# Kernel tuning notes

Hardware: AMD Instinct MI355X
Metric: run time of the kernel (lower is better)

## Reference

```python
import jax, jax.numpy as jnp
import numpy as np

# Model dims: nSet=48, nItemMax=80, input feat=512,
# D = baseChn*max_channel_ratio = 128 = head_size, H = num_heads = 2.
S, N, DIN = 48, 80, 512
D = 128
H, HS = 2, 128
EPS = 1e-3  # layer_normalization epsilon (non-set-norm branch)

def _w(key, fi, fo):
    return jax.random.normal(key, (fi, fo), jnp.float32) / np.sqrt(fi)

def setup_inputs() -> dict:
    key = jax.random.key(0)
    ks = jax.random.split(key, 20)
    sizes = jax.random.randint(ks[0], (S,), 1, N + 1)
    x = jax.random.normal(ks[1], (S, N, DIN), jnp.float32)
    item_mask = (jnp.arange(N)[None, :] < sizes[:, None]).astype(jnp.float32)
    x = x * item_mask[:, :, None]  # zero-pad invalid items (drives ==0 masks)
    return {
        "x": x,
        "x_size": sizes.astype(jnp.float32),
        # trainable MLP (fc1/fc2/fc3, gelu, no bias)
        "W1": _w(ks[2], DIN, 512),
        "W2": _w(ks[3], 512, 256),
        "W3": _w(ks[4], 256, D),
        # encoder self-attention layer
        "Wq_s": _w(ks[5], D, H * HS),
        "Wk_s": _w(ks[6], D, H * HS),
        "Wv_s": _w(ks[7], D, H * HS),
        "Wh_s": _w(ks[8], H * HS, HS),
        "Wfc_e": _w(ks[9], D, D),
        # decoder cross-set attention layer
        "Wq_c": _w(ks[10], D, H * HS),
        "Wk_c": _w(ks[11], D, H * HS),
        "Wv_c": _w(ks[12], D, H * HS),
        "Wh_c": _w(ks[13], H * HS, HS),
        "Wfc_d": _w(ks[14], D, D),
        # cross_set_score
        "Wcs": _w(ks[15], D, H * HS),
        "Wcs2": _w(ks[16], H, 1),
    }

def _gelu(z):
    return jax.nn.gelu(z, approximate=False)  # tf.nn.gelu default

def _item_norm(x):
    # layer_normalization with is_set_norm=False: per-item LN, zero padded rows
    mean = jnp.mean(x, axis=-1, keepdims=True)
    std = jnp.std(x, axis=-1, keepdims=True)
    norm = (x - mean) / (std + EPS)
    keep = jnp.sum(x, axis=-1, keepdims=True) != 0
    return jnp.where(keep, norm, jnp.zeros_like(x))

def _masked_softmax(s):
    # faithful to source: mask entries where raw score == 0
    m = s != 0
    e = jnp.where(m, jnp.exp(s - jnp.max(s, axis=-1, keepdims=True)), 0.0)
    return e / (jnp.sum(e, axis=-1, keepdims=True) + 1e-10)

def _mha(q_in, kv_in, Wq, Wk, Wv, Wh):
    # q_in/kv_in: [S, S, N, D]
    q = (q_in @ Wq).reshape(S, S, N, H, HS)
    k = (kv_in @ Wk).reshape(S, S, N, H, HS)
    v = (kv_in @ Wv).reshape(S, S, N, H, HS)
    s = jnp.einsum('xynhd,xymhd->xyhnm', q, k) / np.sqrt(HS)
    a = _masked_softmax(s)
    o = jnp.einsum('xyhnm,xymhd->xynhd', a, v).reshape(S, S, N, H * HS)
    return o @ Wh  # -> [S, S, N, HS]

def reference(x, x_size, W1, W2, W3, Wq_s, Wk_s, Wv_s, Wh_s, Wfc_e,
              Wq_c, Wk_c, Wv_c, Wh_c, Wfc_d, Wcs, Wcs2):
    # item-wise MLP projection: feat -> 512 -> 256 -> 128
    h = _gelu(_gelu(_gelu(x @ W1) @ W2) @ W3)  # [S, N, D]
    # pairwise set grid [nSet_x, nSet_y, nItemMax, D]
    x4 = jnp.broadcast_to(h[:, None], (S, S, N, D))
    # encoder: self-attention over items within each (i,j) pair
    z = _item_norm(x4)
    x4 = x4 + _mha(z, z, Wq_s, Wk_s, Wv_s, Wh_s)
    z = _item_norm(x4)
    x4 = x4 + _gelu(z @ Wfc_e)
    # decoder: cross-set attention, out[i,j] = Attn(q=z[i,j], kv=z[j,i])
    z = _item_norm(x4)
    x4 = x4 + _mha(z, jnp.transpose(z, (1, 0, 2, 3)), Wq_c, Wk_c, Wv_c, Wh_c)
    z = _item_norm(x4)
    x4 = x4 + _gelu(z @ Wfc_d)
    # cross_set_score: pairwise ReLU-matmul, set-size normalized
    xh = (x4 @ Wcs).reshape(S, S, N, H, HS).transpose(0, 1, 3, 2, 4)  # [j,i,h,n,d]
    A = jax.nn.relu(jnp.einsum('jihnd,ijhmd->jihnm', xh, xh) / np.sqrt(HS))
    sc = A.sum((-1, -2)) / x_size[None, :, None] / x_size[:, None, None]  # [S,S,H]
    return sc @ Wcs2  # [S, S, 1]
```

## Files before the change

kernel.cpp:

```cpp
#include <hip/hip_runtime.h>
#include <hip/hip_bf16.h>


#define SS 48
#define NI 80

typedef unsigned short us;
typedef __attribute__((ext_vector_type(8))) short s8v;
typedef __attribute__((ext_vector_type(4))) float f4v;

#define MFMA(a,b,c) __builtin_amdgcn_mfma_f32_16x16x32_bf16((a),(b),(c),0,0,0)

__device__ __forceinline__ float gelu_f(float x){
  return 0.5f * x * (1.0f + erff(x * 0.7071067811865475f));
}
__device__ __forceinline__ us f2b(float f){
  __hip_bfloat16 b = __float2bfloat16(f);
  return reinterpret_cast<us&>(b);
}
__device__ __forceinline__ s8v zero8(){ s8v v = {0,0,0,0,0,0,0,0}; return v; }
__device__ __forceinline__ void gl16(const void* g, void* l){
  __builtin_amdgcn_global_load_lds(
      (const __attribute__((address_space(1))) void*)g,
      (__attribute__((address_space(3))) void*)l, 16, 0, 0);
}

template<int ABF16, int OUTF32>
__global__ __launch_bounds__(256) void mgemm_k(const void* __restrict__ Ap,
    const float* __restrict__ B, void* __restrict__ Cp, int N, int K)
{
  __shared__ __align__(16) char lds[10240];
  char* As = lds; char* Bs = lds + 5120;
  const int t = threadIdx.x;
  const int wv = t >> 6, lm = t & 15, lh = (t >> 4) & 3;
  const int bx = blockIdx.x, by = blockIdx.y;
  const int ar = wv*16 + lm, r0 = wv*16 + lh*4;
  f4v acc[4];
#pragma unroll
  for (int ct = 0; ct < 4; ++ct) acc[ct] = {0.f,0.f,0.f,0.f};
  const int rA = t >> 2, kcA = (t & 3) << 3;
  const int kkB = t >> 3, nnB = (t & 7) << 3;
  for (int k0 = 0; k0 < K; k0 += 32) {
    __syncthreads();
    if (ABF16) {
      s8v v = *(const s8v*)((const us*)Ap + (size_t)(by*64 + rA)*K + k0 + kcA);
      *(s8v*)(As + rA*80 + kcA*2) = v;
    } else {
      const float* ap = (const float*)Ap + (size_t)(by*64 + rA)*K + k0 + kcA;
      float4 v0 = *(const float4*)ap, v1 = *(const float4*)(ap + 4);
      us tmp[8] = {f2b(v0.x),f2b(v0.y),f2b(v0.z),f2b(v0.w),
                   f2b(v1.x),f2b(v1.y),f2b(v1.z),f2b(v1.w)};
      *(s8v*)(As + rA*80 + kcA*2) = *(const s8v*)tmp;
    }
    {
      const float* bp = B + (size_t)(k0 + kkB)*N + bx*64 + nnB;
      float4 w0 = *(const float4*)bp, w1 = *(const float4*)(bp + 4);
      float w8[8] = {w0.x,w0.y,w0.z,w0.w,w1.x,w1.y,w1.z,w1.w};
#pragma unroll
      for (int q = 0; q < 8; ++q)
        *(us*)(Bs + (nnB + q)*80 + kkB*2) = f2b(w8[q]);
    }
    __syncthreads();
    s8v af = *(const s8v*)(As + ar*80 + lh*16);
#pragma unroll
    for (int ct = 0; ct < 4; ++ct) {
      s8v bf = *(const s8v*)(Bs + (ct*16 + lm)*80 + lh*16);
      acc[ct] = MFMA(af, bf, acc[ct]);
    }
  }
#pragma unroll
  for (int ct = 0; ct < 4; ++ct)
#pragma unroll
    for (int reg = 0; reg < 4; ++reg) {
      size_t r = by*64 + r0 + reg;
      int c = bx*64 + ct*16 + lm;
      float v = gelu_f(acc[ct][reg]);
      if (OUTF32) ((float*)Cp)[r*N + c] = v;
      else ((us*)Cp)[r*N + c] = f2b(v);
    }
}

__global__ __launch_bounds__(256) void qkv_k(const us* __restrict__ A,
    const float* __restrict__ Wq, const float* __restrict__ Wk,
    const float* __restrict__ Wv, us* __restrict__ Qb, us* __restrict__ Kb,
    us* __restrict__ VT)
{
  __shared__ __align__(16) char lds[10240];
  char* As = lds; char* Bs = lds + 5120;
  const int t = threadIdx.x;
  const int wv = t >> 6, lm = t & 15, lh = (t >> 4) & 3;
  const int bx = blockIdx.x, by = blockIdx.y;
  const int sel = bx >> 2, bxx = bx & 3;
  const float* B = sel == 0 ? Wq : (sel == 1 ? Wk : Wv);
  const int ar = wv*16 + lm, r0 = wv*16 + lh*4;
  f4v acc[4];
#pragma unroll
  for (int ct = 0; ct < 4; ++ct) acc[ct] = {0.f,0.f,0.f,0.f};
  const int rA = t >> 2, kcA = (t & 3) << 3;
  const int kkB = t >> 3, nnB = (t & 7) << 3;
#pragma unroll
  for (int k0 = 0; k0 < 128; k0 += 32) {
    __syncthreads();
    {
      s8v v = *(const s8v*)(A + (size_t)(by*64 + rA)*128 + k0 + kcA);
      *(s8v*)(As + rA*80 + kcA*2) = v;
      const float* bp = B + (size_t)(k0 + kkB)*256 + bxx*64 + nnB;
      float4 w0 = *(const float4*)bp, w1 = *(const float4*)(bp + 4);
      float w8[8] = {w0.x,w0.y,w0.z,w0.w,w1.x,w1.y,w1.z,w1.w};
#pragma unroll
      for (int q = 0; q < 8; ++q)
        *(us*)(Bs + (nnB + q)*80 + kkB*2) = f2b(w8[q]);
    }
    __syncthreads();
    s8v af = *(const s8v*)(As + ar*80 + lh*16);
#pragma unroll
    for (int ct = 0; ct < 4; ++ct) {
      s8v bf = *(const s8v*)(Bs + (ct*16 + lm)*80 + lh*16);
      acc[ct] = MFMA(af, bf, acc[ct]);
    }
  }
  if (sel < 2) {
    us* O = sel ? Kb : Qb;
#pragma unroll
    for (int ct = 0; ct < 4; ++ct)
#pragma unroll
      for (int reg = 0; reg < 4; ++reg)
        O[(size_t)(by*64 + r0 + reg)*256 + bxx*64 + ct*16 + lm] = f2b(acc[ct][reg]);
  } else {
#pragma unroll
    for (int ct = 0; ct < 4; ++ct)
#pragma unroll
      for (int reg = 0; reg < 4; ++reg) {
        int r = by*64 + r0 + reg;
        int s = r / 80, m = r % 80;
        int d = bxx*64 + ct*16 + lm;
        VT[((size_t)s*256 + d)*80 + m] = f2b(acc[ct][reg]);
      }
  }
}

__global__ __launch_bounds__(64) void norm_k(const float* __restrict__ in,
                                             us* __restrict__ out)
{
  const int r = blockIdx.x, t = threadIdx.x;
  float v0 = in[(size_t)r*128 + t];
  float v1 = in[(size_t)r*128 + t + 64];
  float sm = v0 + v1;
#pragma unroll
  for (int off = 1; off < 64; off <<= 1) sm += __shfl_xor(sm, off, 64);
  float mean = sm * (1.0f/128.0f);
  float d0 = v0 - mean, d1 = v1 - mean;
  float vs = d0*d0 + d1*d1;
#pragma unroll
  for (int off = 1; off < 64; off <<= 1) vs += __shfl_xor(vs, off, 64);
  float inv = 1.0f / (sqrtf(vs * (1.0f/128.0f)) + 1e-3f);
  bool keep = (sm != 0.0f);
  out[(size_t)r*128 + t]      = f2b(keep ? d0*inv : 0.0f);
  out[(size_t)r*128 + t + 64] = f2b(keep ? d1*inv : 0.0f);
}

__global__ __launch_bounds__(128) void prep_k(
    const float* __restrict__ Wh_s, const float* __restrict__ Wfc_e,
    const float* __restrict__ Wh_c, const float* __restrict__ Wfc_d,
    const float* __restrict__ Wcs,  const float* __restrict__ Wv_s,
    const float* __restrict__ Wv_c,
    us* __restrict__ WfcTe, us* __restrict__ WfcTd,
    float* __restrict__ Wvh_s, float* __restrict__ Wvh_c,
    us* __restrict__ Mb)
{
  const int x = blockIdx.x, task = blockIdx.y, tid = threadIdx.x;
  if (task == 0) {
    WfcTe[x*128 + tid] = f2b(Wfc_e[(size_t)tid*128 + x]);
  } else if (task == 1) {
    WfcTd[x*128 + tid] = f2b(Wfc_d[(size_t)tid*128 + x]);
  } else if (task < 6) {
    int h = (task - 2) & 1;
    const float* Wv = task < 4 ? Wv_s : Wv_c;
    const float* Wh = task < 4 ? Wh_s : Wh_c;
    float* Wvh = task < 4 ? Wvh_s : Wvh_c;
    float acc = 0.f;
#pragma unroll 8
    for (int d = 0; d < 128; ++d)
      acc = fmaf(Wv[(size_t)x*256 + h*128 + d], Wh[(size_t)(h*128 + d)*128 + tid], acc);
    Wvh[(size_t)x*256 + h*128 + tid] = acc;
  } else {
    int h = task - 6;
    float acc = 0.f;
#pragma unroll 8
    for (int k = 0; k < 128; ++k)
      acc = fmaf(Wcs[(size_t)x*256 + h*128 + k], Wcs[(size_t)tid*256 + h*128 + k], acc);
    Mb[(size_t)h*16384 + x*128 + tid] = f2b(acc);
  }
}

template<int PERM_RES>
__device__ __forceinline__ void attn4(int a, int b, int t,
    const us* __restrict__ Qg, const us* __restrict__ Kg,
    const us* __restrict__ VTg, const float* __restrict__ baseg,
    const us* __restrict__ WfcT,
    char* __restrict__ X, char* __restrict__ Y, f4v x4[8])
{
  const int wv = t >> 6, lane = t & 63, lm = t & 15, lh = (t >> 4) & 3;
  const int ar = wv*16 + lm, r0 = wv*16 + lh*4;
  const float isq = 0.08838834764831845f;
#pragma unroll
  for (int dt = 0; dt < 8; ++dt) x4[dt] = (f4v){0.f,0.f,0.f,0.f};

#pragma unroll 1
  for (int h = 0; h < 2; ++h) {
    if (h == 1) __syncthreads();
#pragma unroll
    for (int c = 0; c < 4; ++c) {
      int chunk = wv*4 + c;
      int row = chunk*4 + (lane >> 4);
      int scb = ((lane & 15) << 4) ^ ((row & 7) << 4);
      gl16(Kg + (((size_t)(b*NI + row)) << 8) + h*128 + (scb >> 1), X + chunk*1024);
    }
    s8v qf[4];
    {
      const us* qrow = Qg + (((size_t)(a*NI + ar)) << 8) + h*128 + lh*8;
#pragma unroll
      for (int ks = 0; ks < 4; ++ks) qf[ks] = *(const s8v*)(qrow + ks*32);
    }
    __syncthreads();
    f4v sA[5];
#pragma unroll
    for (int nt = 0; nt < 5; ++nt) {
      int row = nt*16 + lm;
      f4v acc = (f4v){0.f,0.f,0.f,0.f};
#pragma unroll
      for (int ks = 0; ks < 4; ++ks) {
        s8v kf = *(const s8v*)(X + row*256 + ((ks*64 + lh*16) ^ ((row & 7) << 4)));
        acc = MFMA(qf[ks], kf, acc);
      }
      sA[nt] = acc;
    }
#pragma unroll
    for (int reg = 0; reg < 4; ++reg) {
      int r = r0 + reg;
      float sv[5];
#pragma unroll
      for (int nt = 0; nt < 5; ++nt) sv[nt] = sA[nt][reg] * isq;
      float mx = sv[0];
#pragma unroll
      for (int nt = 1; nt < 5; ++nt) mx = fmaxf(mx, sv[nt]);
#pragma unroll
      for (int off = 1; off < 16; off <<= 1) mx = fmaxf(mx, __shfl_xor(mx, off, 64));
      float e[5], sum = 0.f;
#pragma unroll
      for (int nt = 0; nt < 5; ++nt) {
        e[nt] = (sv[nt] != 0.f) ? __expf(sv[nt] - mx) : 0.f;
        sum += e[nt];
      }
#pragma unroll
      for (int off = 1; off < 16; off <<= 1) sum += __shfl_xor(sum, off, 64);
      float inv = 1.f / (sum + 1e-10f);
#pragma unroll
      for (int nt = 0; nt < 5; ++nt)
        *(us*)(Y + r*256 + ((2*(nt*16 + lm)) ^ ((r & 7) << 4))) = f2b(e[nt] * inv);
    }
    s8v pf0 = *(const s8v*)(Y + ar*256 + ((lh*16) ^ ((ar & 7) << 4)));
    s8v pf1 = *(const s8v*)(Y + ar*256 + ((64 + lh*16) ^ ((ar & 7) << 4)));
    s8v pf2 = zero8();
    if (lh < 2)
      pf2 = *(const s8v*)(Y + ar*256 + ((128 + lh*16) ^ ((ar & 7) << 4)));
    __syncthreads();
#pragma unroll
    for (int c = 0; c < 4; ++c) {
      int chunk = wv*4 + c;
      int L = chunk*1024 + lane*16;
      int rv = L / 160;
      int rem = L - rv*160;
      int cv = (rem >> 4) - (rv % 10); if (cv < 0) cv += 10;
      gl16(VTg + ((size_t)(b*256 + h*128 + rv))*80 + (cv << 3), X + chunk*1024);
    }
    __syncthreads();
#pragma unroll
    for (int dt = 0; dt < 8; ++dt) {
      int row = dt*16 + lm;
      int rm = (row % 10) << 4;
      int o0 = lh*16 + rm; if (o0 >= 160) o0 -= 160;
      x4[dt] = MFMA(pf0, *(const s8v*)(X + row*160 + o0), x4[dt]);
      int o1 = 64 + lh*16 + rm; if (o1 >= 160) o1 -= 160;
      x4[dt] = MFMA(pf1, *(const s8v*)(X + row*160 + o1), x4[dt]);
      s8v v2 = zero8();
      if (lh < 2) {
        int o2 = 128 + lh*16 + rm; if (o2 >= 160) o2 -= 160;
        v2 = *(const s8v*)(X + row*160 + o2);
      }
      x4[dt] = MFMA(pf2, v2, x4[dt]);
    }
    if (h == 1) {
      if (PERM_RES) {
#pragma unroll
        for (int reg = 0; reg < 4; ++reg) {
          const f4v* bp = (const f4v*)(baseg + (((size_t)(a*NI + r0 + reg)) << 7) + lm*8);
          f4v b0 = bp[0], b1 = bp[1];
#pragma unroll
          for (int dt = 0; dt < 4; ++dt) {
            x4[dt][reg]   += b0[dt];
            x4[dt+4][reg] += b1[dt];
          }
        }
      } else {
#pragma unroll
        for (int reg = 0; reg < 4; ++reg) {
          int r = r0 + reg;
#pragma unroll
          for (int dt = 0; dt < 8; ++dt)
            x4[dt][reg] += baseg[(((size_t)(a*NI + r)) << 7) + dt*16 + lm];
        }
      }
    }
  }

  __syncthreads();
  for (int chunk = wv; chunk < 16; chunk += 5) {
    int row = chunk*4 + (lane >> 4);
    int scb = ((lane & 15) << 4) ^ ((row & 7) << 4);
    gl16(WfcT + (size_t)row*128 + (scb >> 1), X + chunk*1024);
  }
#pragma unroll
  for (int reg = 0; reg < 4; ++reg) {
    int r = r0 + reg;
    float sm = 0.f;
#pragma unroll
    for (int dt = 0; dt < 8; ++dt) sm += x4[dt][reg];
#pragma unroll
    for (int off = 1; off < 16; off <<= 1) sm += __shfl_xor(sm, off, 64);
    float mean = sm * (1.0f/128.0f);
    float vs = 0.f;
#pragma unroll
    for (int dt = 0; dt < 8; ++dt) { float d = x4[dt][reg] - mean; vs = fmaf(d, d, vs); }
#pragma unroll
    for (int off = 1; off < 16; off <<= 1) vs += __shfl_xor(vs, off, 64);
    float inv = 1.f / (sqrtf(vs * (1.0f/128.0f)) + 1e-3f);
    bool keep = (sm != 0.f);
#pragma unroll
    for (int dt = 0; dt < 8; ++dt)
      *(us*)(Y + r*256 + ((2*(dt*16 + lm)) ^ ((r & 7) << 4))) = f2b(keep ? (x4[dt][reg]-mean)*inv : 0.f);
  }
  s8v zf[4];
#pragma unroll
  for (int ks = 0; ks < 4; ++ks)
    zf[ks] = *(const s8v*)(Y + ar*256 + ((ks*64 + lh*16) ^ ((ar & 7) << 4)));
  __syncthreads();
#pragma unroll
  for (int dt = 0; dt < 4; ++dt) {
    int row = dt*16 + lm;
    f4v acc = (f4v){0.f,0.f,0.f,0.f};
#pragma unroll
    for (int ks = 0; ks < 4; ++ks) {
      s8v wfr = *(const s8v*)(X + row*256 + ((ks*64 + lh*16) ^ ((row & 7) << 4)));
      acc = MFMA(zf[ks], wfr, acc);
    }
#pragma unroll
    for (int reg = 0; reg < 4; ++reg) x4[dt][reg] += gelu_f(acc[reg]);
  }
  __syncthreads();
  for (int chunk = wv; chunk < 16; chunk += 5) {
    int row = chunk*4 + (lane >> 4);
    int scb = ((lane & 15) << 4) ^ ((row & 7) << 4);
    gl16(WfcT + (size_t)(row + 64)*128 + (scb >> 1), X + chunk*1024);
  }
  __syncthreads();
#pragma unroll
  for (int dt = 4; dt < 8; ++dt) {
    int row = dt*16 + lm;
    int r2 = row - 64;
    f4v acc = (f4v){0.f,0.f,0.f,0.f};
#pragma unroll
    for (int ks = 0; ks < 4; ++ks) {
      s8v wfr = *(const s8v*)(X + r2*256 + ((ks*64 + lh*16) ^ ((row & 7) << 4)));
      acc = MFMA(zf[ks], wfr, acc);
    }
#pragma unroll
    for (int reg = 0; reg < 4; ++reg) x4[dt][reg] += gelu_f(acc[reg]);
  }
}

__global__ __launch_bounds__(320) void enc_k(
    const us* __restrict__ Qg, const us* __restrict__ Kg,
    const us* __restrict__ VTg, const float* __restrict__ hb,
    const us* __restrict__ WfcT, float* __restrict__ e2p,
    us* __restrict__ z3b)
{
  __shared__ __align__(16) char X[20480];
  __shared__ __align__(16) char Y[20480];
  const int t = threadIdx.x;
  const int wv = t >> 6, lm = t & 15, lh = (t >> 4) & 3;
  const int r0 = wv*16 + lh*4;
  const int i = blockIdx.x;
  f4v x4[8];
  attn4<0>(i, i, t, Qg, Kg, VTg, hb, WfcT, X, Y, x4);
#pragma unroll
  for (int reg = 0; reg < 4; ++reg) {
    int r = r0 + reg;
    size_t gb = ((size_t)(i*NI + r)) << 7;
    float tmp[8]; float sm = 0.f;
#pragma unroll
    for (int dt = 0; dt < 8; ++dt) { tmp[dt] = x4[dt][reg]; sm += tmp[dt]; }
    *(float4*)(e2p + gb + lm*8)     = make_float4(tmp[0],tmp[1],tmp[2],tmp[3]);
    *(float4*)(e2p + gb + lm*8 + 4) = make_float4(tmp[4],tmp[5],tmp[6],tmp[7]);
#pragma unroll
    for (int off = 1; off < 16; off <<= 1) sm += __shfl_xor(sm, off, 64);
    float mean = sm * (1.0f/128.0f);
    float vs = 0.f;
#pragma unroll
    for (int dt = 0; dt < 8; ++dt) { float d = tmp[dt] - mean; vs = fmaf(d, d, vs); }
#pragma unroll
    for (int off = 1; off < 16; off <<= 1) vs += __shfl_xor(vs, off, 64);
    float inv = 1.f / (sqrtf(vs * (1.0f/128.0f)) + 1e-3f);
    bool keep = (sm != 0.f);
#pragma unroll
    for (int dt = 0; dt < 8; ++dt)
      z3b[gb + dt*16 + lm] = f2b(keep ? (tmp[dt]-mean)*inv : 0.f);
  }
}

__global__ __launch_bounds__(320) void dec_k(
    const us* __restrict__ Qg, const us* __restrict__ Kg,
    const us* __restrict__ VTg, const float* __restrict__ e2p,
    const us* __restrict__ WfcT, us* __restrict__ x4g)
{
  __shared__ __align__(16) char X[20480];
  __shared__ __align__(16) char Y[20480];
  const int t = threadIdx.x;
  const int wv = t >> 6, lane = t & 63, lm = t & 15, lh = (t >> 4) & 3;
  const int r0 = wv*16 + lh*4;
  const int a = blockIdx.x, b = blockIdx.y;
  f4v x4[8];
  attn4<1>(a, b, t, Qg, Kg, VTg, e2p, WfcT, X, Y, x4);
#pragma unroll
  for (int reg = 0; reg < 4; ++reg) {
    int r = r0 + reg;
#pragma unroll
    for (int dt = 0; dt < 8; ++dt)
      *(us*)(Y + r*256 + ((2*(dt*16 + lm)) ^ ((r & 7) << 4))) = f2b(x4[dt][reg]);
  }
  const size_t pid = (size_t)a*SS + b;
  char* dst = (char*)(x4g + pid*10240);
#pragma unroll
  for (int q = 0; q < 4; ++q) {
    int c = lane + q*64;
    int row = wv*16 + (c >> 4);
    int cb = (c & 15) << 4;
    s8v v = *(const s8v*)(Y + row*256 + (cb ^ ((row & 7) << 4)));
    *(s8v*)(dst + row*256 + cb) = v;
  }
}

__global__ __launch_bounds__(320) void ugemm2_k(const us* __restrict__ x4g,
    const us* __restrict__ Mb, us* __restrict__ Ugc)
{
  __shared__ __align__(16) char As[20480];
  __shared__ __align__(16) char Bs[16384];
  const int t = threadIdx.x;
  const int wv = t >> 6, lane = t & 63, lm = t & 15, lh = (t >> 4) & 3;
  const int ar = wv*16 + lm, r0 = wv*16 + lh*4;
  int bid = blockIdx.x;
  int ii = (int)(0.5f*(97.0f - sqrtf(9409.0f - 8.0f*(float)bid)));
  if (ii > 47) ii = 47; if (ii < 0) ii = 0;
  while (ii*SS - ii*(ii-1)/2 > bid) --ii;
  while ((ii+1)*SS - (ii+1)*ii/2 <= bid) ++ii;
  const int i = ii, j = ii + (bid - (ii*SS - ii*(ii-1)/2));
  const us* A = x4g + ((size_t)j*SS + i)*10240;

#pragma unroll
  for (int c = 0; c < 4; ++c) {
    int chunk = wv*4 + c;
    int row = chunk*4 + (lane >> 4);
    int scb = ((lane & 15) << 4) ^ ((row & 7) << 4);
    gl16(A + (size_t)row*128 + (scb >> 1), As + chunk*1024);
  }
  f4v acc[16];
#pragma unroll
  for (int ct = 0; ct < 16; ++ct) acc[ct] = (f4v){0.f,0.f,0.f,0.f};
#pragma unroll 1
  for (int k0 = 0; k0 < 128; k0 += 32) {
    if (k0) __syncthreads();
    for (int c = wv; c < 16; c += 5) {
      int row = c*16 + (lane >> 2);
      int colb = (lane & 3) << 4;
      int scb = colb ^ ((row & 3) << 4);
      gl16(Mb + (size_t)row*128 + k0 + (scb >> 1), Bs + c*1024);
    }
    __syncthreads();
    int ks = k0 >> 5;
    s8v af = *(const s8v*)(As + ar*256 + ((ks*64 + lh*16) ^ ((ar & 7) << 4)));
#pragma unroll
    for (int ct = 0; ct < 16; ++ct) {
      int row = ct*16 + lm;
      s8v bf = *(const s8v*)(Bs + row*64 + ((lh*16) ^ ((row & 3) << 4)));
      acc[ct] = MFMA(af, bf, acc[ct]);
    }
  }
#pragma unroll
  for (int ct = 0; ct < 16; ++ct)
#pragma unroll
    for (int reg = 0; reg < 4; ++reg)
      Ugc[((size_t)bid*80 + r0 + reg)*256 + ct*16 + lm] = f2b(acc[ct][reg]);
}

__global__ __launch_bounds__(320) void p3_k(
    const us* __restrict__ x4g, const us* __restrict__ Ugc,
    const float* __restrict__ Wcs2, const float* __restrict__ xsg,
    float* __restrict__ outg)
{
  __shared__ __align__(16) char Xi[20480];
  __shared__ __align__(16) char Xu[20480];
  __shared__ float red[10];
  const int t = threadIdx.x;
  const int wv = t >> 6, lane = t & 63, lm = t & 15, lh = (t >> 4) & 3;
  const int ar = wv*16 + lm, r0 = wv*16 + lh*4;
  const float isq = 0.08838834764831845f;

  int bid0 = blockIdx.x;
  int bid = (bid0 & 7) * 147 + (bid0 >> 3);
  int ii = (int)(0.5f*(97.0f - sqrtf(9409.0f - 8.0f*(float)bid)));
  if (ii > 47) ii = 47; if (ii < 0) ii = 0;
  while (ii*SS - ii*(ii-1)/2 > bid) --ii;
  while ((ii+1)*SS - (ii+1)*ii/2 <= bid) ++ii;
  const int i = ii, j = ii + (bid - (ii*SS - ii*(ii-1)/2));
  const size_t xpid = (size_t)i*SS + j;

#pragma unroll
  for (int c = 0; c < 4; ++c) {
    int chunk = wv*4 + c;
    int row = chunk*4 + (lane >> 4);
    int scb = ((lane & 15) << 4) ^ ((row & 7) << 4);
    gl16(x4g + xpid*10240 + (size_t)row*128 + (scb >> 1), Xi + chunk*1024);
    gl16(Ugc + ((size_t)bid*80 + row)*256 + (scb >> 1), Xu + chunk*1024);
  }
  __syncthreads();
  s8v xf[4];
#pragma unroll
  for (int ks = 0; ks < 4; ++ks)
    xf[ks] = *(const s8v*)(Xi + ar*256 + ((ks*64 + lh*16) ^ ((ar & 7) << 4)));

  float sc[2];
#pragma unroll 1
  for (int h = 0; h < 2; ++h) {
    if (h == 1) {
      __syncthreads();
#pragma unroll
      for (int c = 0; c < 4; ++c) {
        int chunk = wv*4 + c;
        int row = chunk*4 + (lane >> 4);
        int scb = ((lane & 15) << 4) ^ ((row & 7) << 4);
        gl16(Ugc + ((size_t)bid*80 + row)*256 + 128 + (scb >> 1), Xu + chunk*1024);
      }
      __syncthreads();
    }
    float loc = 0.f;
#pragma unroll
    for (int nt = 0; nt < 5; ++nt) {
      int brow = nt*16 + lm;
      f4v acc = (f4v){0.f,0.f,0.f,0.f};
#pragma unroll
      for (int ks = 0; ks < 4; ++ks) {
        s8v bf = *(const s8v*)(Xu + brow*256 + ((ks*64 + lh*16) ^ ((brow & 7) << 4)));
        acc = MFMA(xf[ks], bf, acc);
      }
#pragma unroll
      for (int reg = 0; reg < 4; ++reg) loc += fmaxf(acc[reg]*isq, 0.f);
    }
    sc[h] = loc;
  }
#pragma unroll
  for (int off = 1; off < 64; off <<= 1) {
    sc[0] += __shfl_xor(sc[0], off, 64);
    sc[1] += __shfl_xor(sc[1], off, 64);
  }
  if ((t & 63) == 0) { red[wv] = sc[0]; red[wv + 5] = sc[1]; }
  __syncthreads();
  if (t == 0) {
    float s0 = red[0]+red[1]+red[2]+red[3]+red[4];
    float s1 = red[5]+red[6]+red[7]+red[8]+red[9];
    float val = (s0*Wcs2[0] + s1*Wcs2[1]) / (xsg[i]*xsg[j]);
    outg[i*SS + j] = val;
    outg[j*SS + i] = val;
  }
}

extern "C" void kernel_launch(void* const* d_in, const int* in_sizes, int n_in,
                              void* d_out, int out_size, void* d_ws, size_t ws_size,
                              hipStream_t stream)
{
  (void)in_sizes; (void)n_in; (void)out_size; (void)ws_size;
  const float* x     = (const float*)d_in[0];
  const float* xs    = (const float*)d_in[1];
  const float* W1    = (const float*)d_in[2];
  const float* W2    = (const float*)d_in[3];
  const float* W3    = (const float*)d_in[4];
  const float* Wq_s  = (const float*)d_in[5];
  const float* Wk_s  = (const float*)d_in[6];
  const float* Wv_s  = (const float*)d_in[7];
  const float* Wh_s  = (const float*)d_in[8];
  const float* Wfc_e = (const float*)d_in[9];
  const float* Wq_c  = (const float*)d_in[10];
  const float* Wk_c  = (const float*)d_in[11];
  const float* Wv_c  = (const float*)d_in[12];
  const float* Wh_c  = (const float*)d_in[13];
  const float* Wfc_d = (const float*)d_in[14];
  const float* Wcs   = (const float*)d_in[15];
  const float* Wcs2  = (const float*)d_in[16];
  float* out = (float*)d_out;

  char* w = (char*)d_ws;
  us* h1b     = (us*)w;    w += (size_t)3840*512*2;
  us* h2b     = (us*)w;    w += (size_t)3840*256*2;
  float* hb   = (float*)w; w += (size_t)3840*128*4;
  us* zb16    = (us*)w;    w += (size_t)3840*128*2;
  us* z3b     = (us*)w;    w += (size_t)3840*128*2;
  float* e2p  = (float*)w; w += (size_t)3840*128*4;
  us* Qb      = (us*)w;    w += (size_t)3840*256*2;
  us* Kb      = (us*)w;    w += (size_t)3840*256*2;
  us* VT      = (us*)w;    w += (size_t)48*256*80*2;
  us* WfcTe   = (us*)w;    w += 16384*2;
  us* WfcTd   = (us*)w;    w += 16384*2;
  us* Mb      = (us*)w;    w += 32768*2;
  float* Wvh_s = (float*)w; w += 32768*4;
  float* Wvh_c = (float*)w; w += 32768*4;
  us* x4g     = (us*)w;    w += (size_t)2304*10240*2;
  us* Ugc     = (us*)w;    w += (size_t)1176*80*256*2;

  hipLaunchKernelGGL(prep_k, dim3(128, 8), dim3(128), 0, stream,
                     Wh_s, Wfc_e, Wh_c, Wfc_d, Wcs, Wv_s, Wv_c,
                     WfcTe, WfcTd, Wvh_s, Wvh_c, Mb);
  hipLaunchKernelGGL((mgemm_k<0,0>), dim3(8,60), dim3(256), 0, stream,
                     (const void*)x, W1, (void*)h1b, 512, 512);
  hipLaunchKernelGGL((mgemm_k<1,0>), dim3(4,60), dim3(256), 0, stream,
                     (const void*)h1b, W2, (void*)h2b, 256, 512);
  hipLaunchKernelGGL((mgemm_k<1,1>), dim3(2,60), dim3(256), 0, stream,
                     (const void*)h2b, W3, (void*)hb, 128, 256);
  hipLaunchKernelGGL(norm_k, dim3(3840), dim3(64), 0, stream, hb, zb16);
  hipLaunchKernelGGL(qkv_k, dim3(12,60), dim3(256), 0, stream,
                     zb16, Wq_s, Wk_s, Wvh_s, Qb, Kb, VT);
  hipLaunchKernelGGL(enc_k, dim3(48), dim3(320), 0, stream,
                     Qb, Kb, VT, hb, WfcTe, e2p, z3b);
  hipLaunchKernelGGL(qkv_k, dim3(12,60), dim3(256), 0, stream,
                     z3b, Wq_c, Wk_c, Wvh_c, Qb, Kb, VT);
  hipLaunchKernelGGL(dec_k, dim3(48,48), dim3(320), 0, stream,
                     Qb, Kb, VT, e2p, WfcTd, x4g);
  hipLaunchKernelGGL(ugemm2_k, dim3(1176), dim3(320), 0, stream, x4g, Mb, Ugc);
  hipLaunchKernelGGL(p3_k, dim3(1176), dim3(320), 0, stream,
                     x4g, Ugc, Wcs2, xs, out);
}
```

Baseline: 286.8 us.

## Rewrite decoder kernel with double-buffered staging and two pairs per block

```diff
diff --git a/kernel.cpp b/kernel.cpp
--- a/kernel.cpp
+++ b/kernel.cpp
@@ -291,25 +291,12 @@
       x4[dt] = MFMA(pf2, v2, x4[dt]);
     }
     if (h == 1) {
-      if (PERM_RES) {
-#pragma unroll
-        for (int reg = 0; reg < 4; ++reg) {
-          const f4v* bp = (const f4v*)(baseg + (((size_t)(a*NI + r0 + reg)) << 7) + lm*8);
-          f4v b0 = bp[0], b1 = bp[1];
-#pragma unroll
-          for (int dt = 0; dt < 4; ++dt) {
-            x4[dt][reg]   += b0[dt];
-            x4[dt+4][reg] += b1[dt];
-          }
-        }
-      } else {
-#pragma unroll
-        for (int reg = 0; reg < 4; ++reg) {
-          int r = r0 + reg;
-#pragma unroll
-          for (int dt = 0; dt < 8; ++dt)
-            x4[dt][reg] += baseg[(((size_t)(a*NI + r)) << 7) + dt*16 + lm];
-        }
+#pragma unroll
+      for (int reg = 0; reg < 4; ++reg) {
+        int r = r0 + reg;
+#pragma unroll
+        for (int dt = 0; dt < 8; ++dt)
+          x4[dt][reg] += baseg[(((size_t)(a*NI + r)) << 7) + dt*16 + lm];
       }
     }
   }
@@ -418,35 +405,216 @@
   }
 }
 
-__global__ __launch_bounds__(320) void dec_k(
+__global__ __launch_bounds__(320) void dec3_k(
     const us* __restrict__ Qg, const us* __restrict__ Kg,
     const us* __restrict__ VTg, const float* __restrict__ e2p,
     const us* __restrict__ WfcT, us* __restrict__ x4g)
 {
-  __shared__ __align__(16) char X[20480];
+  __shared__ __align__(16) char S0[20480];
+  __shared__ __align__(16) char S1[20480];
   __shared__ __align__(16) char Y[20480];
   const int t = threadIdx.x;
   const int wv = t >> 6, lane = t & 63, lm = t & 15, lh = (t >> 4) & 3;
-  const int r0 = wv*16 + lh*4;
-  const int a = blockIdx.x, b = blockIdx.y;
-  f4v x4[8];
-  attn4<1>(a, b, t, Qg, Kg, VTg, e2p, WfcT, X, Y, x4);
-#pragma unroll
-  for (int reg = 0; reg < 4; ++reg) {
-    int r = r0 + reg;
-#pragma unroll
-    for (int dt = 0; dt < 8; ++dt)
-      *(us*)(Y + r*256 + ((2*(dt*16 + lm)) ^ ((r & 7) << 4))) = f2b(x4[dt][reg]);
-  }
-  const size_t pid = (size_t)a*SS + b;
-  char* dst = (char*)(x4g + pid*10240);
-#pragma unroll
-  for (int q = 0; q < 4; ++q) {
-    int c = lane + q*64;
-    int row = wv*16 + (c >> 4);
-    int cb = (c & 15) << 4;
-    s8v v = *(const s8v*)(Y + row*256 + (cb ^ ((row & 7) << 4)));
-    *(s8v*)(dst + row*256 + cb) = v;
+  const int ar = wv*16 + lm, r0 = wv*16 + lh*4;
+  const float isq = 0.08838834764831845f;
+  const int a = blockIdx.x;
+  const int b0 = blockIdx.y * 2;
+
+  auto stgK = [&](char* D, int b, int h) {
+#pragma unroll
+    for (int c = 0; c < 4; ++c) {
+      int chunk = wv*4 + c;
+      int row = chunk*4 + (lane >> 4);
+      int scb = ((lane & 15) << 4) ^ ((row & 7) << 4);
+      gl16(Kg + (((size_t)(b*NI + row)) << 8) + h*128 + (scb >> 1), D + chunk*1024);
+    }
+  };
+  auto stgVT = [&](char* D, int b, int h) {
+#pragma unroll
+    for (int c = 0; c < 4; ++c) {
+      int chunk = wv*4 + c;
+      int L = chunk*1024 + lane*16;
+      int rv = L / 160;
+      int cv = ((L - rv*160) >> 4) - (rv % 10); if (cv < 0) cv += 10;
+      gl16(VTg + ((size_t)(b*256 + h*128 + rv))*80 + (cv << 3), D + chunk*1024);
+    }
+  };
+  auto stgW = [&](char* D, int half) {
+    for (int chunk = wv; chunk < 16; chunk += 5) {
+      int row = chunk*4 + (lane >> 4);
+      int scb = ((lane & 15) << 4) ^ ((row & 7) << 4);
+      gl16(WfcT + (size_t)(row + half*64)*128 + (scb >> 1), D + chunk*1024);
+    }
+  };
+  auto qksm = [&](const char* KS, int h, s8v& pf0, s8v& pf1, s8v& pf2) {
+    s8v qf[4];
+    {
+      const us* qrow = Qg + (((size_t)(a*NI + ar)) << 8) + h*128 + lh*8;
+#pragma unroll
+      for (int ks = 0; ks < 4; ++ks) qf[ks] = *(const s8v*)(qrow + ks*32);
+    }
+    f4v sA[5];
+#pragma unroll
+    for (int nt = 0; nt < 5; ++nt) {
+      int row = nt*16 + lm;
+      f4v acc = (f4v){0.f,0.f,0.f,0.f};
+#pragma unroll
+      for (int ks = 0; ks < 4; ++ks) {
+        s8v kf = *(const s8v*)(KS + row*256 + ((ks*64 + lh*16) ^ ((row & 7) << 4)));
+        acc = MFMA(qf[ks], kf, acc);
+      }
+      sA[nt] = acc;
+    }
+#pragma unroll
+    for (int reg = 0; reg < 4; ++reg) {
+      int r = r0 + reg;
+      float sv[5];
+#pragma unroll
+      for (int nt = 0; nt < 5; ++nt) sv[nt] = sA[nt][reg] * isq;
+      float mx = sv[0];
+#pragma unroll
+      for (int nt = 1; nt < 5; ++nt) mx = fmaxf(mx, sv[nt]);
+#pragma unroll
+      for (int off = 1; off < 16; off <<= 1) mx = fmaxf(mx, __shfl_xor(mx, off, 64));
+      float e[5], sum = 0.f;
+#pragma unroll
+      for (int nt = 0; nt < 5; ++nt) {
+        e[nt] = (sv[nt] != 0.f) ? __expf(sv[nt] - mx) : 0.f;
+        sum += e[nt];
+      }
+#pragma unroll
+      for (int off = 1; off < 16; off <<= 1) sum += __shfl_xor(sum, off, 64);
+      float inv = 1.f / (sum + 1e-10f);
+#pragma unroll
+      for (int nt = 0; nt < 5; ++nt)
+        *(us*)(Y + r*256 + ((2*(nt*16 + lm)) ^ ((r & 7) << 4))) = f2b(e[nt] * inv);
+    }
+    pf0 = *(const s8v*)(Y + ar*256 + ((lh*16) ^ ((ar & 7) << 4)));
+    pf1 = *(const s8v*)(Y + ar*256 + ((64 + lh*16) ^ ((ar & 7) << 4)));
+    pf2 = zero8();
+    if (lh < 2)
+      pf2 = *(const s8v*)(Y + ar*256 + ((128 + lh*16) ^ ((ar & 7) << 4)));
+  };
+  auto pv = [&](const char* VS, s8v pf0, s8v pf1, s8v pf2, f4v* x4) {
+#pragma unroll
+    for (int dt = 0; dt < 8; ++dt) {
+      int row = dt*16 + lm;
+      int rm = (row % 10) << 4;
+      int o0 = lh*16 + rm; if (o0 >= 160) o0 -= 160;
+      x4[dt] = MFMA(pf0, *(const s8v*)(VS + row*160 + o0), x4[dt]);
+      int o1 = 64 + lh*16 + rm; if (o1 >= 160) o1 -= 160;
+      x4[dt] = MFMA(pf1, *(const s8v*)(VS + row*160 + o1), x4[dt]);
+      s8v v2 = zero8();
+      if (lh < 2) {
+        int o2 = 128 + lh*16 + rm; if (o2 >= 160) o2 -= 160;
+        v2 = *(const s8v*)(VS + row*160 + o2);
+      }
+      x4[dt] = MFMA(pf2, v2, x4[dt]);
+    }
+  };
+
+  stgK(S0, b0, 0);
+
+#pragma unroll 1
+  for (int bi = 0; bi < 2; ++bi) {
+    const int b = b0 + bi;
+    f4v x4[8];
+#pragma unroll
+    for (int dt = 0; dt < 8; ++dt) x4[dt] = (f4v){0.f,0.f,0.f,0.f};
+    s8v pf0, pf1, pf2, zf[4];
+
+    __syncthreads();
+    stgVT(S1, b, 0);
+    qksm(S0, 0, pf0, pf1, pf2);
+    __syncthreads();
+    stgK(S0, b, 1);
+    pv(S1, pf0, pf1, pf2, x4);
+    __syncthreads();
+    stgVT(S1, b, 1);
+    qksm(S0, 1, pf0, pf1, pf2);
+    __syncthreads();
+    stgW(S0, 0);
+    pv(S1, pf0, pf1, pf2, x4);
+#pragma unroll
+    for (int reg = 0; reg < 4; ++reg) {
+      const f4v* bp = (const f4v*)(e2p + (((size_t)(a*NI + r0 + reg)) << 7) + lm*8);
+      f4v bb0 = bp[0], bb1 = bp[1];
+#pragma unroll
+      for (int dt = 0; dt < 4; ++dt) {
+        x4[dt][reg]   += bb0[dt];
+        x4[dt+4][reg] += bb1[dt];
+      }
+    }
+    __syncthreads();
+    stgW(S1, 1);
+#pragma unroll
+    for (int reg = 0; reg < 4; ++reg) {
+      int r = r0 + reg;
+      float sm = 0.f;
+#pragma unroll
+      for (int dt = 0; dt < 8; ++dt) sm += x4[dt][reg];
+#pragma unroll
+      for (int off = 1; off < 16; off <<= 1) sm += __shfl_xor(sm, off, 64);
+      float mean = sm * (1.0f/128.0f);
+      float vs = 0.f;
+#pragma unroll
+      for (int dt = 0; dt < 8; ++dt) { float d = x4[dt][reg] - mean; vs = fmaf(d, d, vs); }
+#pragma unroll
+      for (int off = 1; off < 16; off <<= 1) vs += __shfl_xor(vs, off, 64);
+      float inv = 1.f / (sqrtf(vs * (1.0f/128.0f)) + 1e-3f);
+      bool keep = (sm != 0.f);
+#pragma unroll
+      for (int dt = 0; dt < 8; ++dt)
+        *(us*)(Y + r*256 + ((2*(dt*16 + lm)) ^ ((r & 7) << 4))) = f2b(keep ? (x4[dt][reg]-mean)*inv : 0.f);
+    }
+#pragma unroll
+    for (int ks = 0; ks < 4; ++ks)
+      zf[ks] = *(const s8v*)(Y + ar*256 + ((ks*64 + lh*16) ^ ((ar & 7) << 4)));
+#pragma unroll
+    for (int dt = 0; dt < 4; ++dt) {
+      int row = dt*16 + lm;
+      f4v acc = (f4v){0.f,0.f,0.f,0.f};
+#pragma unroll
+      for (int ks = 0; ks < 4; ++ks) {
+        s8v wfr = *(const s8v*)(S0 + row*256 + ((ks*64 + lh*16) ^ ((row & 7) << 4)));
+        acc = MFMA(zf[ks], wfr, acc);
+      }
+#pragma unroll
+      for (int reg = 0; reg < 4; ++reg) x4[dt][reg] += gelu_f(acc[reg]);
+    }
+    __syncthreads();
+    if (bi == 0) stgK(S0, b0 + 1, 0);
+#pragma unroll
+    for (int dt = 4; dt < 8; ++dt) {
+      int row = dt*16 + lm;
+      int r2 = row - 64;
+      f4v acc = (f4v){0.f,0.f,0.f,0.f};
+#pragma unroll
+      for (int ks = 0; ks < 4; ++ks) {
+        s8v wfr = *(const s8v*)(S1 + r2*256 + ((ks*64 + lh*16) ^ ((row & 7) << 4)));
+        acc = MFMA(zf[ks], wfr, acc);
+      }
+#pragma unroll
+      for (int reg = 0; reg < 4; ++reg) x4[dt][reg] += gelu_f(acc[reg]);
+    }
+#pragma unroll
+    for (int reg = 0; reg < 4; ++reg) {
+      int r = r0 + reg;
+#pragma unroll
+      for (int dt = 0; dt < 8; ++dt)
+        *(us*)(Y + r*256 + ((2*(dt*16 + lm)) ^ ((r & 7) << 4))) = f2b(x4[dt][reg]);
+    }
+    {
+      char* dst = (char*)(x4g + ((size_t)a*SS + b)*10240);
+#pragma unroll
+      for (int q = 0; q < 4; ++q) {
+        int c = lane + q*64;
+        int row = wv*16 + (c >> 4);
+        int cb = (c & 15) << 4;
+        s8v v = *(const s8v*)(Y + row*256 + (cb ^ ((row & 7) << 4)));
+        *(s8v*)(dst + row*256 + cb) = v;
+      }
+    }
   }
 }
 
@@ -641,7 +809,7 @@
                      Qb, Kb, VT, hb, WfcTe, e2p, z3b);
   hipLaunchKernelGGL(qkv_k, dim3(12,60), dim3(256), 0, stream,
                      z3b, Wq_c, Wk_c, Wvh_c, Qb, Kb, VT);
-  hipLaunchKernelGGL(dec_k, dim3(48,48), dim3(320), 0, stream,
+  hipLaunchKernelGGL(dec3_k, dim3(48,24), dim3(320), 0, stream,
                      Qb, Kb, VT, e2p, WfcTd, x4g);
   hipLaunchKernelGGL(ugemm2_k, dim3(1176), dim3(320), 0, stream, x4g, Mb, Ugc);
   hipLaunchKernelGGL(p3_k, dim3(1176), dim3(320), 0, stream,
```

Result: slower. 363.3 us (+26.7%).

## Double-buffer LDS in decoder attention to overlap K/V/W staging with compute

Applied to the files above, without the earlier changes.

```diff
diff --git a/kernel.cpp b/kernel.cpp
--- a/kernel.cpp
+++ b/kernel.cpp
@@ -193,8 +193,7 @@
   }
 }
 
-template<int PERM_RES>
-__device__ __forceinline__ void attn4(int a, int b, int t,
+__device__ __forceinline__ void attn4e(int a, int t,
     const us* __restrict__ Qg, const us* __restrict__ Kg,
     const us* __restrict__ VTg, const float* __restrict__ baseg,
     const us* __restrict__ WfcT,
@@ -203,6 +202,7 @@
   const int wv = t >> 6, lane = t & 63, lm = t & 15, lh = (t >> 4) & 3;
   const int ar = wv*16 + lm, r0 = wv*16 + lh*4;
   const float isq = 0.08838834764831845f;
+  const int b = a;
 #pragma unroll
   for (int dt = 0; dt < 8; ++dt) x4[dt] = (f4v){0.f,0.f,0.f,0.f};
 
@@ -291,25 +291,12 @@
       x4[dt] = MFMA(pf2, v2, x4[dt]);
     }
     if (h == 1) {
-      if (PERM_RES) {
-#pragma unroll
-        for (int reg = 0; reg < 4; ++reg) {
-          const f4v* bp = (const f4v*)(baseg + (((size_t)(a*NI + r0 + reg)) << 7) + lm*8);
-          f4v b0 = bp[0], b1 = bp[1];
-#pragma unroll
-          for (int dt = 0; dt < 4; ++dt) {
-            x4[dt][reg]   += b0[dt];
-            x4[dt+4][reg] += b1[dt];
-          }
-        }
-      } else {
-#pragma unroll
-        for (int reg = 0; reg < 4; ++reg) {
-          int r = r0 + reg;
-#pragma unroll
-          for (int dt = 0; dt < 8; ++dt)
-            x4[dt][reg] += baseg[(((size_t)(a*NI + r)) << 7) + dt*16 + lm];
-        }
+#pragma unroll
+      for (int reg = 0; reg < 4; ++reg) {
+        int r = r0 + reg;
+#pragma unroll
+        for (int dt = 0; dt < 8; ++dt)
+          x4[dt][reg] += baseg[(((size_t)(a*NI + r)) << 7) + dt*16 + lm];
       }
     }
   }
@@ -392,7 +379,7 @@
   const int r0 = wv*16 + lh*4;
   const int i = blockIdx.x;
   f4v x4[8];
-  attn4<0>(i, i, t, Qg, Kg, VTg, hb, WfcT, X, Y, x4);
+  attn4e(i, t, Qg, Kg, VTg, hb, WfcT, X, Y, x4);
 #pragma unroll
   for (int reg = 0; reg < 4; ++reg) {
     int r = r0 + reg;
@@ -418,36 +405,185 @@
   }
 }
 
-__global__ __launch_bounds__(320) void dec_k(
+__global__ __launch_bounds__(320) void dec4_k(
     const us* __restrict__ Qg, const us* __restrict__ Kg,
     const us* __restrict__ VTg, const float* __restrict__ e2p,
     const us* __restrict__ WfcT, us* __restrict__ x4g)
 {
-  __shared__ __align__(16) char X[20480];
+  __shared__ __align__(16) char S0[20480];
+  __shared__ __align__(16) char S1[20480];
   __shared__ __align__(16) char Y[20480];
   const int t = threadIdx.x;
   const int wv = t >> 6, lane = t & 63, lm = t & 15, lh = (t >> 4) & 3;
-  const int r0 = wv*16 + lh*4;
+  const int ar = wv*16 + lm, r0 = wv*16 + lh*4;
+  const float isq = 0.08838834764831845f;
   const int a = blockIdx.x, b = blockIdx.y;
+
+#define STG_K(DST, H)                                                        \
+  { _Pragma("unroll") for (int c_ = 0; c_ < 4; ++c_) {                       \
+      int ch_ = wv*4 + c_;                                                   \
+      int rw_ = ch_*4 + (lane >> 4);                                         \
+      int sc_ = ((lane & 15) << 4) ^ ((rw_ & 7) << 4);                       \
+      gl16(Kg + (((size_t)(b*NI + rw_)) << 8) + (H)*128 + (sc_ >> 1),        \
+           (DST) + ch_*1024); } }
+#define STG_VT(DST, H)                                                       \
+  { _Pragma("unroll") for (int c_ = 0; c_ < 4; ++c_) {                       \
+      int ch_ = wv*4 + c_;                                                   \
+      int L_ = ch_*1024 + lane*16;                                           \
+      int rv_ = L_ / 160;                                                    \
+      int cv_ = ((L_ - rv_*160) >> 4) - (rv_ % 10); if (cv_ < 0) cv_ += 10;  \
+      gl16(VTg + ((size_t)(b*256 + (H)*128 + rv_))*80 + (cv_ << 3),          \
+           (DST) + ch_*1024); } }
+#define STG_W(DST, HALF)                                                     \
+  { for (int ch_ = wv; ch_ < 16; ch_ += 5) {                                 \
+      int rw_ = ch_*4 + (lane >> 4);                                         \
+      int sc_ = ((lane & 15) << 4) ^ ((rw_ & 7) << 4);                       \
+      gl16(WfcT + (size_t)(rw_ + (HALF)*64)*128 + (sc_ >> 1),                \
+           (DST) + ch_*1024); } }
+#define QKSM(KS, H)                                                          \
+  { s8v qf_[4];                                                              \
+    { const us* qr_ = Qg + (((size_t)(a*NI + ar)) << 8) + (H)*128 + lh*8;    \
+      _Pragma("unroll") for (int ks = 0; ks < 4; ++ks)                       \
+        qf_[ks] = *(const s8v*)(qr_ + ks*32); }                              \
+    f4v sA_[5];                                                              \
+    _Pragma("unroll") for (int nt = 0; nt < 5; ++nt) {                       \
+      int rw_ = nt*16 + lm;                                                  \
+      f4v ac_ = (f4v){0.f,0.f,0.f,0.f};                                      \
+      _Pragma("unroll") for (int ks = 0; ks < 4; ++ks) {                     \
+        s8v kf_ = *(const s8v*)((KS) + rw_*256 +                             \
+                                ((ks*64 + lh*16) ^ ((rw_ & 7) << 4)));       \
+        ac_ = MFMA(qf_[ks], kf_, ac_); }                                     \
+      sA_[nt] = ac_; }                                                       \
+    _Pragma("unroll") for (int reg = 0; reg < 4; ++reg) {                    \
+      int r_ = r0 + reg;                                                     \
+      float sv_[5];                                                          \
+      _Pragma("unroll") for (int nt = 0; nt < 5; ++nt)                       \
+        sv_[nt] = sA_[nt][reg] * isq;                                        \
+      float mx_ = sv_[0];                                                    \
+      _Pragma("unroll") for (int nt = 1; nt < 5; ++nt)                       \
+        mx_ = fmaxf(mx_, sv_[nt]);                                           \
+      _Pragma("unroll") for (int of_ = 1; of_ < 16; of_ <<= 1)               \
+        mx_ = fmaxf(mx_, __shfl_xor(mx_, of_, 64));                          \
+      float e_[5], su_ = 0.f;                                                \
+      _Pragma("unroll") for (int nt = 0; nt < 5; ++nt) {                     \
+        e_[nt] = (sv_[nt] != 0.f) ? __expf(sv_[nt] - mx_) : 0.f;             \
+        su_ += e_[nt]; }                                                     \
+      _Pragma("unroll") for (int of_ = 1; of_ < 16; of_ <<= 1)               \
+        su_ += __shfl_xor(su_, of_, 64);                                     \
+      float iv_ = 1.f / (su_ + 1e-10f);                                      \
+      _Pragma("unroll") for (int nt = 0; nt < 5; ++nt)                       \
+        *(us*)(Y + r_*256 + ((2*(nt*16 + lm)) ^ ((r_ & 7) << 4))) =          \
+            f2b(e_[nt] * iv_); } }
+#define PV(VS)                                                               \
+  { s8v pf0_ = *(const s8v*)(Y + ar*256 + ((lh*16) ^ ((ar & 7) << 4)));      \
+    s8v pf1_ = *(const s8v*)(Y + ar*256 + ((64 + lh*16) ^ ((ar & 7) << 4))); \
+    s8v pf2_ = zero8();                                                      \
+    if (lh < 2)                                                              \
+      pf2_ = *(const s8v*)(Y + ar*256 + ((128 + lh*16) ^ ((ar & 7) << 4)));  \
+    _Pragma("unroll") for (int dt = 0; dt < 8; ++dt) {                       \
+      int rw_ = dt*16 + lm;                                                  \
+      int rm_ = (rw_ % 10) << 4;                                             \
+      int o0_ = lh*16 + rm_; if (o0_ >= 160) o0_ -= 160;                     \
+      x4[dt] = MFMA(pf0_, *(const s8v*)((VS) + rw_*160 + o0_), x4[dt]);      \
+      int o1_ = 64 + lh*16 + rm_; if (o1_ >= 160) o1_ -= 160;                \
+      x4[dt] = MFMA(pf1_, *(const s8v*)((VS) + rw_*160 + o1_), x4[dt]);      \
+      s8v v2_ = zero8();                                                     \
+      if (lh < 2) { int o2_ = 128 + lh*16 + rm_;                             \
+        if (o2_ >= 160) o2_ -= 160;                                          \
+        v2_ = *(const s8v*)((VS) + rw_*160 + o2_); }                         \
+      x4[dt] = MFMA(pf2_, v2_, x4[dt]); } }
+#define FCH(WS, D0)                                                          \
+  { s8v zf_[4];                                                              \
+    _Pragma("unroll") for (int ks = 0; ks < 4; ++ks)                         \
+      zf_[ks] = *(const s8v*)(Y + ar*256 +                                   \
+                              ((ks*64 + lh*16) ^ ((ar & 7) << 4)));          \
+    _Pragma("unroll") for (int dt = (D0); dt < (D0)+4; ++dt) {               \
+      int rw_ = dt*16 + lm;                                                  \
+      int rl_ = rw_ - (D0)*16;                                               \
+      f4v ac_ = (f4v){0.f,0.f,0.f,0.f};                                      \
+      _Pragma("unroll") for (int ks = 0; ks < 4; ++ks) {                     \
+        s8v wf_ = *(const s8v*)((WS) + rl_*256 +                             \
+                                ((ks*64 + lh*16) ^ ((rw_ & 7) << 4)));       \
+        ac_ = MFMA(zf_[ks], wf_, ac_); }                                     \
+      _Pragma("unroll") for (int reg = 0; reg < 4; ++reg)                    \
+        x4[dt][reg] += gelu_f(ac_[reg]); } }
+
   f4v x4[8];
-  attn4<1>(a, b, t, Qg, Kg, VTg, e2p, WfcT, X, Y, x4);
+#pragma unroll
+  for (int dt = 0; dt < 8; ++dt) x4[dt] = (f4v){0.f,0.f,0.f,0.f};
+
+  STG_K(S0, 0);
+  __syncthreads();
+  STG_VT(S1, 0);
+  QKSM(S0, 0);
+  __syncthreads();
+  STG_K(S0, 1);
+  PV(S1);
+  __syncthreads();
+  STG_VT(S1, 1);
+  QKSM(S0, 1);
+  __syncthreads();
+  STG_W(S0, 0);
+  PV(S1);
+#pragma unroll
+  for (int reg = 0; reg < 4; ++reg) {
+    const f4v* bp = (const f4v*)(e2p + (((size_t)(a*NI + r0 + reg)) << 7) + lm*8);
+    f4v bb0 = bp[0], bb1 = bp[1];
+#pragma unroll
+    for (int dt = 0; dt < 4; ++dt) {
+      x4[dt][reg]   += bb0[dt];
+      x4[dt+4][reg] += bb1[dt];
+    }
+  }
+  __syncthreads();
+  STG_W(S1, 1);
 #pragma unroll
   for (int reg = 0; reg < 4; ++reg) {
     int r = r0 + reg;
+    float sm = 0.f;
+#pragma unroll
+    for (int dt = 0; dt < 8; ++dt) sm += x4[dt][reg];
+#pragma unroll
+    for (int off = 1; off < 16; off <<= 1) sm += __shfl_xor(sm, off, 64);
+    float mean = sm * (1.0f/128.0f);
+    float vs = 0.f;
+#pragma unroll
+    for (int dt = 0; dt < 8; ++dt) { float d = x4[dt][reg] - mean; vs = fmaf(d, d, vs); }
+#pragma unroll
+    for (int off = 1; off < 16; off <<= 1) vs += __shfl_xor(vs, off, 64);
+    float inv = 1.f / (sqrtf(vs * (1.0f/128.0f)) + 1e-3f);
+    bool keep = (sm != 0.f);
+#pragma unroll
+    for (int dt = 0; dt < 8; ++dt)
+      *(us*)(Y + r*256 + ((2*(dt*16 + lm)) ^ ((r & 7) << 4))) = f2b(keep ? (x4[dt][reg]-mean)*inv : 0.f);
+  }
+  FCH(S0, 0);
+  __syncthreads();
+  FCH(S1, 4);
+#pragma unroll
+  for (int reg = 0; reg < 4; ++reg) {
+    int r = r0 + reg;
 #pragma unroll
     for (int dt = 0; dt < 8; ++dt)
       *(us*)(Y + r*256 + ((2*(dt*16 + lm)) ^ ((r & 7) << 4))) = f2b(x4[dt][reg]);
   }
-  const size_t pid = (size_t)a*SS + b;
-  char* dst = (char*)(x4g + pid*10240);
-#pragma unroll
-  for (int q = 0; q < 4; ++q) {
-    int c = lane + q*64;
-    int row = wv*16 + (c >> 4);
-    int cb = (c & 15) << 4;
-    s8v v = *(const s8v*)(Y + row*256 + (cb ^ ((row & 7) << 4)));
-    *(s8v*)(dst + row*256 + cb) = v;
-  }
+  {
+    char* dst = (char*)(x4g + ((size_t)a*SS + b)*10240);
+#pragma unroll
+    for (int q = 0; q < 4; ++q) {
+      int c = lane + q*64;
+      int row = wv*16 + (c >> 4);
+      int cb = (c & 15) << 4;
+      s8v v = *(const s8v*)(Y + row*256 + (cb ^ ((row & 7) << 4)));
+      *(s8v*)(dst + row*256 + cb) = v;
+    }
+  }
+#undef STG_K
+#undef STG_VT
+#undef STG_W
+#undef QKSM
+#undef PV
+#undef FCH
 }
 
 __global__ __launch_bounds__(320) void ugemm2_k(const us* __restrict__ x4g,
@@ -641,7 +777,7 @@
                      Qb, Kb, VT, hb, WfcTe, e2p, z3b);
   hipLaunchKernelGGL(qkv_k, dim3(12,60), dim3(256), 0, stream,
                      z3b, Wq_c, Wk_c, Wvh_c, Qb, Kb, VT);
-  hipLaunchKernelGGL(dec_k, dim3(48,48), dim3(320), 0, stream,
+  hipLaunchKernelGGL(dec4_k, dim3(48,48), dim3(320), 0, stream,
                      Qb, Kb, VT, e2p, WfcTd, x4g);
   hipLaunchKernelGGL(ugemm2_k, dim3(1176), dim3(320), 0, stream, x4g, Mb, Ugc);
   hipLaunchKernelGGL(p3_k, dim3(1176), dim3(320), 0, stream,
```

Result: faster. 280.7 us (-2.2%).
